# Kernel optimization log

Measured on AMD Instinct MI355X. Metric: run time of the kernel, lower is better.

Reference implementation:

```python
import jax, jax.numpy as jnp
import numpy as np

N_QUBITS = 4
CHROMOSOME = [["rx_gate", "ry_gate", "rz_gate", "h_gate"],
              ["cnot_gate", "cnot_gate", "cnot_gate", "cnot_gate"],
              ["ry_gate", "ry_gate", "ry_gate", "ry_gate"]]

_H = (jnp.array([[1.0, 1.0], [1.0, -1.0]], dtype=jnp.complex64) / jnp.sqrt(2.0).astype(jnp.complex64))


def _ry(t):
    c = jnp.cos(t / 2).astype(jnp.complex64)
    s = jnp.sin(t / 2).astype(jnp.complex64)
    return jnp.stack([jnp.stack([c, -s], -1), jnp.stack([s, c], -1)], -2)


def _rx(t):
    c = jnp.cos(t / 2).astype(jnp.complex64)
    s = (-1j) * jnp.sin(t / 2).astype(jnp.complex64)
    return jnp.stack([jnp.stack([c, s], -1), jnp.stack([s, c], -1)], -2)


def _rz(t):
    e = jnp.exp(-1j * t.astype(jnp.complex64) / 2)
    z = jnp.zeros_like(e)
    return jnp.stack([jnp.stack([e, z], -1), jnp.stack([z, jnp.conj(e)], -1)], -2)


def _apply_1q(state, U, q):
    # state: [N, 2,2,...,2]; U: [2,2] (shared) or [N,2,2] (per-patch encoding)
    s = jnp.moveaxis(state, 1 + q, -1)
    if U.ndim == 3:
        s = jnp.einsum('nab,n...b->n...a', U, s)
    else:
        s = jnp.einsum('ab,n...b->n...a', U, s)
    return jnp.moveaxis(s, -1, 1 + q)


def _cnot(state, c, t):
    s = jnp.moveaxis(state, (1 + c, 1 + t), (-2, -1))
    # control=0 slice unchanged; control=1 slice gets X on target (flip last axis)
    s = jnp.concatenate([s[..., 0:1, :], s[..., 1:2, ::-1]], axis=-2)
    return jnp.moveaxis(s, (-2, -1), (1 + c, 1 + t))


def _simulate(patches, params):
    # patches: [N, n_qubits] real angles in [0,1); params: [n_params]
    N = patches.shape[0]
    state = jnp.zeros((N, 2 ** N_QUBITS), dtype=jnp.complex64).at[:, 0].set(1.0)
    state = state.reshape((N,) + (2,) * N_QUBITS)
    # angle encoding: RY(pi * x_q) on qubit q (encoder='ry' for multichannel path)
    for q in range(N_QUBITS):
        state = _apply_1q(state, _ry(jnp.pi * patches[:, q]), q)
    idx = 0
    for layer in CHROMOSOME:
        for q, g in enumerate(layer):
            if g == 'rx_gate':
                state = _apply_1q(state, _rx(params[idx]), q); idx += 1
            elif g == 'ry_gate':
                state = _apply_1q(state, _ry(params[idx]), q); idx += 1
            elif g == 'rz_gate':
                state = _apply_1q(state, _rz(params[idx]), q); idx += 1
            elif g == 'h_gate':
                state = _apply_1q(state, _H, q)
            elif g == 'cnot_gate':
                state = _cnot(state, q, (q + 1) % N_QUBITS)
    probs = state.real ** 2 + state.imag ** 2  # [N, 2,2,2,2]
    exps = []
    for q in range(N_QUBITS):
        p = jnp.sum(probs, axis=tuple(a for a in range(1, 1 + N_QUBITS) if a != 1 + q))  # [N,2]
        exps.append(p[:, 0] - p[:, 1])  # <Z_q>
    return jnp.stack(exps, -1)  # [N, n_qubits]


def setup_inputs() -> dict:
    key = jax.random.key(0)
    k1, k2 = jax.random.split(key)
    x = jax.random.uniform(k1, (2048, 3, 196, 4), dtype=jnp.float32)
    ansatz_params = jax.random.uniform(k2, (7,), dtype=jnp.float32) * jnp.pi
    return {"x": x, "ansatz_params": ansatz_params}


def reference(x, ansatz_params):
    B, C, P, D = x.shape
    out = _simulate(x.reshape(-1, D), ansatz_params)  # [B*C*P, n_qubits]
    out = out.reshape(B, C, P, N_QUBITS)
    image_size = int((P * N_QUBITS) ** 0.5)  # 28
    # faithful to torch .view(n_images, image_size, image_size, n_channels)
    return out.reshape(B, image_size, image_size, C)
```

## Files before the change

### kernel.cpp

```cpp
#include <hip/hip_runtime.h>


__global__ __launch_bounds__(256) void quanv_kernel(
    const float* __restrict__ x,
    const float* __restrict__ prm,
    float* __restrict__ out,
    int n)
{
    int tid = blockIdx.x * 256 + threadIdx.x;
    if (tid >= n) return;

    float S0, C0, S1, C1, S2, C2;
    __sincosf(prm[0] * 0.5f, &S0, &C0);
    __sincosf(prm[1] * 0.5f, &S1, &C1);
    __sincosf(prm[2] * 0.5f, &S2, &C2);
    float Sf0, Cf0, Sf1, Cf1, Sf2, Cf2, Sf3, Cf3;
    __sincosf(prm[3], &Sf0, &Cf0);
    __sincosf(prm[4], &Sf1, &Cf1);
    __sincosf(prm[5], &Sf2, &Cf2);
    __sincosf(prm[6], &Sf3, &Cf3);

    const float4 xv = reinterpret_cast<const float4*>(x)[tid];

    const float HPI = 1.5707963267948966f;
    float e0s, e0c, e1s, e1c, e2s, e2c, e3s, e3c;
    __sincosf(xv.x * HPI, &e0s, &e0c);
    __sincosf(xv.y * HPI, &e1s, &e1c);
    __sincosf(xv.z * HPI, &e2s, &e2c);
    __sincosf(xv.w * HPI, &e3s, &e3c);

    float v00r = C0 * e0c, v00i = -S0 * e0s;
    float v01r = C0 * e0s, v01i = -S0 * e0c;
    float v10 = C1 * e1c - S1 * e1s;
    float v11 = S1 * e1c + C1 * e1s;
    float v20r = e2c * C2, v20i = -e2c * S2;
    float v21r = e2s * C2, v21i =  e2s * S2;
    const float RS2 = 0.70710678118654752f;
    float v30 = (e3c + e3s) * RS2;
    float v31 = (e3c - e3s) * RS2;

    float t00r = v00r * v10, t00i = v00i * v10;
    float t01r = v00r * v11, t01i = v00i * v11;
    float t10r = v01r * v10, t10i = v01i * v10;
    float t11r = v01r * v11, t11i = v01i * v11;
    float u00r = v20r * v30, u00i = v20i * v30;
    float u01r = v20r * v31, u01i = v20i * v31;
    float u10r = v21r * v30, u10i = v21i * v30;
    float u11r = v21r * v31, u11i = v21i * v31;

#define CMUL(dr, di, ar, ai, br, bi) \
    float dr = (ar) * (br) - (ai) * (bi); \
    float di = (ar) * (bi) + (ai) * (br);
    CMUL(a0r, a0i,  t00r, t00i, u00r, u00i)
    CMUL(a1r, a1i,  t11r, t11i, u01r, u01i)
    CMUL(a2r, a2i,  t00r, t00i, u11r, u11i)
    CMUL(a3r, a3i,  t11r, t11i, u10r, u10i)
    CMUL(a4r, a4i,  t01r, t01i, u10r, u10i)
    CMUL(a5r, a5i,  t10r, t10i, u11r, u11i)
    CMUL(a6r, a6i,  t01r, t01i, u01r, u01i)
    CMUL(a7r, a7i,  t10r, t10i, u00r, u00i)
    CMUL(a8r, a8i,  t11r, t11i, u00r, u00i)
    CMUL(a9r, a9i,  t00r, t00i, u01r, u01i)
    CMUL(a10r, a10i, t11r, t11i, u11r, u11i)
    CMUL(a11r, a11i, t00r, t00i, u10r, u10i)
    CMUL(a12r, a12i, t10r, t10i, u10r, u10i)
    CMUL(a13r, a13i, t01r, t01i, u11r, u11i)
    CMUL(a14r, a14i, t10r, t10i, u01r, u01i)
    CMUL(a15r, a15i, t01r, t01i, u00r, u00i)
#undef CMUL

#define PROB(k) float p##k = a##k##r * a##k##r + a##k##i * a##k##i;
    PROB(0) PROB(1) PROB(2) PROB(3) PROB(4) PROB(5) PROB(6) PROB(7)
    PROB(8) PROB(9) PROB(10) PROB(11) PROB(12) PROB(13) PROB(14) PROB(15)
#undef PROB

    float zpA = (p0 + p1) + (p2 + p3);
    float zpB = (p4 + p5) + (p6 + p7);
    float zpC = (p8 + p9) + (p10 + p11);
    float zpD = (p12 + p13) + (p14 + p15);
    float z0 = (zpA + zpB) - (zpC + zpD);
    float z1 = (zpA + zpC) - (zpB + zpD);
    float z2 = ((p0 + p1) + (p4 + p5) + (p8 + p9) + (p12 + p13))
             - ((p2 + p3) + (p6 + p7) + (p10 + p11) + (p14 + p15));
    float z3 = ((p0 + p2) + (p4 + p6) + (p8 + p10) + (p12 + p14))
             - ((p1 + p3) + (p5 + p7) + (p9 + p11) + (p13 + p15));

#define DOT(m, n) (a##m##r * a##n##r + a##m##i * a##n##i)
    float xs0 = DOT(0, 8) + DOT(1, 9) + DOT(2, 10) + DOT(3, 11)
              + DOT(4, 12) + DOT(5, 13) + DOT(6, 14) + DOT(7, 15);
    float xs1 = DOT(0, 4) + DOT(1, 5) + DOT(2, 6) + DOT(3, 7)
              + DOT(8, 12) + DOT(9, 13) + DOT(10, 14) + DOT(11, 15);
    float xs2 = DOT(0, 2) + DOT(1, 3) + DOT(4, 6) + DOT(5, 7)
              + DOT(8, 10) + DOT(9, 11) + DOT(12, 14) + DOT(13, 15);
    float xs3 = DOT(0, 1) + DOT(2, 3) + DOT(4, 5) + DOT(6, 7)
              + DOT(8, 9) + DOT(10, 11) + DOT(12, 13) + DOT(14, 15);
#undef DOT

    float4 o;
    o.x = Cf0 * z0 - 2.0f * Sf0 * xs0;
    o.y = Cf1 * z1 - 2.0f * Sf1 * xs1;
    o.z = Cf2 * z2 - 2.0f * Sf2 * xs2;
    o.w = Cf3 * z3 - 2.0f * Sf3 * xs3;
    reinterpret_cast<float4*>(out)[tid] = o;
}

extern "C" void kernel_launch(void* const* d_in, const int* in_sizes, int n_in,
                              void* d_out, int out_size, void* d_ws, size_t ws_size,
                              hipStream_t stream) {
    const float* x   = (const float*)d_in[0];
    const float* prm = (const float*)d_in[1];
    float* out = (float*)d_out;
    int n = in_sizes[0] / 4;
    int blocks = (n + 255) / 256;
    quanv_kernel<<<blocks, 256, 0, stream>>>(x, prm, out, n);
}
```

Baseline: 77.34 us.

## Replace statevector simulation with closed-form expectation formulas

```diff
diff --git a/kernel.cpp b/kernel.cpp
--- a/kernel.cpp
+++ b/kernel.cpp
@@ -2,114 +2,63 @@
 
 
 __global__ __launch_bounds__(256) void quanv_kernel(
-    const float* __restrict__ x,
+    const float4* __restrict__ x,
     const float* __restrict__ prm,
-    float* __restrict__ out,
+    float4* __restrict__ out,
     int n)
 {
     int tid = blockIdx.x * 256 + threadIdx.x;
     if (tid >= n) return;
 
-    float S0, C0, S1, C1, S2, C2;
-    __sincosf(prm[0] * 0.5f, &S0, &C0);
-    __sincosf(prm[1] * 0.5f, &S1, &C1);
-    __sincosf(prm[2] * 0.5f, &S2, &C2);
-    float Sf0, Cf0, Sf1, Cf1, Sf2, Cf2, Sf3, Cf3;
-    __sincosf(prm[3], &Sf0, &Cf0);
-    __sincosf(prm[4], &Sf1, &Cf1);
-    __sincosf(prm[5], &Sf2, &Cf2);
-    __sincosf(prm[6], &Sf3, &Cf3);
+    const float INV_2PI = 0.15915494309189535f;
 
-    const float4 xv = reinterpret_cast<const float4*>(x)[tid];
+    float A   = __builtin_amdgcn_cosf(prm[0] * INV_2PI);
+    float Cp1 = __builtin_amdgcn_cosf(prm[1] * INV_2PI);
+    float Sp1 = __builtin_amdgcn_sinf(prm[1] * INV_2PI);
+    float Bc  = __builtin_amdgcn_cosf(prm[2] * INV_2PI);
+    float Cf0 = __builtin_amdgcn_cosf(prm[3] * INV_2PI);
+    float Sf0 = __builtin_amdgcn_sinf(prm[3] * INV_2PI);
+    float Cf1 = __builtin_amdgcn_cosf(prm[4] * INV_2PI);
+    float Sf1 = __builtin_amdgcn_sinf(prm[4] * INV_2PI);
+    float Cf2 = __builtin_amdgcn_cosf(prm[5] * INV_2PI);
+    float Sf2 = __builtin_amdgcn_sinf(prm[5] * INV_2PI);
+    float Cf3 = __builtin_amdgcn_cosf(prm[6] * INV_2PI);
+    float Sf3 = __builtin_amdgcn_sinf(prm[6] * INV_2PI);
 
-    const float HPI = 1.5707963267948966f;
-    float e0s, e0c, e1s, e1c, e2s, e2c, e3s, e3c;
-    __sincosf(xv.x * HPI, &e0s, &e0c);
-    __sincosf(xv.y * HPI, &e1s, &e1c);
-    __sincosf(xv.z * HPI, &e2s, &e2c);
-    __sincosf(xv.w * HPI, &e3s, &e3c);
+    const float4 xv = x[tid];
 
-    float v00r = C0 * e0c, v00i = -S0 * e0s;
-    float v01r = C0 * e0s, v01i = -S0 * e0c;
-    float v10 = C1 * e1c - S1 * e1s;
-    float v11 = S1 * e1c + C1 * e1s;
-    float v20r = e2c * C2, v20i = -e2c * S2;
-    float v21r = e2s * C2, v21i =  e2s * S2;
-    const float RS2 = 0.70710678118654752f;
-    float v30 = (e3c + e3s) * RS2;
-    float v31 = (e3c - e3s) * RS2;
+    float c0 = __builtin_amdgcn_cosf(0.5f * xv.x);
+    float s0 = __builtin_amdgcn_sinf(0.5f * xv.x);
+    float c1 = __builtin_amdgcn_cosf(0.5f * xv.y);
+    float s1 = __builtin_amdgcn_sinf(0.5f * xv.y);
+    float c2 = __builtin_amdgcn_cosf(0.5f * xv.z);
+    float s2 = __builtin_amdgcn_sinf(0.5f * xv.z);
+    float c3 = __builtin_amdgcn_cosf(0.5f * xv.w);
+    float s3 = __builtin_amdgcn_sinf(0.5f * xv.w);
 
-    float t00r = v00r * v10, t00i = v00i * v10;
-    float t01r = v00r * v11, t01i = v00i * v11;
-    float t10r = v01r * v10, t10i = v01i * v10;
-    float t11r = v01r * v11, t11i = v01i * v11;
-    float u00r = v20r * v30, u00i = v20i * v30;
-    float u01r = v20r * v31, u01i = v20i * v31;
-    float u10r = v21r * v30, u10i = v21i * v30;
-    float u11r = v21r * v31, u11i = v21i * v31;
+    float z1 = c1 * Cp1 - s1 * Sp1;
+    float x1 = s1 * Cp1 + c1 * Sp1;
 
-#define CMUL(dr, di, ar, ai, br, bi) \
-    float dr = (ar) * (br) - (ai) * (bi); \
-    float di = (ar) * (bi) + (ai) * (br);
-    CMUL(a0r, a0i,  t00r, t00i, u00r, u00i)
-    CMUL(a1r, a1i,  t11r, t11i, u01r, u01i)
-    CMUL(a2r, a2i,  t00r, t00i, u11r, u11i)
-    CMUL(a3r, a3i,  t11r, t11i, u10r, u10i)
-    CMUL(a4r, a4i,  t01r, t01i, u10r, u10i)
-    CMUL(a5r, a5i,  t10r, t10i, u11r, u11i)
-    CMUL(a6r, a6i,  t01r, t01i, u01r, u01i)
-    CMUL(a7r, a7i,  t10r, t10i, u00r, u00i)
-    CMUL(a8r, a8i,  t11r, t11i, u00r, u00i)
-    CMUL(a9r, a9i,  t00r, t00i, u01r, u01i)
-    CMUL(a10r, a10i, t11r, t11i, u11r, u11i)
-    CMUL(a11r, a11i, t00r, t00i, u10r, u10i)
-    CMUL(a12r, a12i, t10r, t10i, u10r, u10i)
-    CMUL(a13r, a13i, t01r, t01i, u11r, u11i)
-    CMUL(a14r, a14i, t10r, t10i, u01r, u01i)
-    CMUL(a15r, a15i, t01r, t01i, u00r, u00i)
-#undef CMUL
-
-#define PROB(k) float p##k = a##k##r * a##k##r + a##k##i * a##k##i;
-    PROB(0) PROB(1) PROB(2) PROB(3) PROB(4) PROB(5) PROB(6) PROB(7)
-    PROB(8) PROB(9) PROB(10) PROB(11) PROB(12) PROB(13) PROB(14) PROB(15)
-#undef PROB
-
-    float zpA = (p0 + p1) + (p2 + p3);
-    float zpB = (p4 + p5) + (p6 + p7);
-    float zpC = (p8 + p9) + (p10 + p11);
-    float zpD = (p12 + p13) + (p14 + p15);
-    float z0 = (zpA + zpB) - (zpC + zpD);
-    float z1 = (zpA + zpC) - (zpB + zpD);
-    float z2 = ((p0 + p1) + (p4 + p5) + (p8 + p9) + (p12 + p13))
-             - ((p2 + p3) + (p6 + p7) + (p10 + p11) + (p14 + p15));
-    float z3 = ((p0 + p2) + (p4 + p6) + (p8 + p10) + (p12 + p14))
-             - ((p1 + p3) + (p5 + p7) + (p9 + p11) + (p13 + p15));
-
-#define DOT(m, n) (a##m##r * a##n##r + a##m##i * a##n##i)
-    float xs0 = DOT(0, 8) + DOT(1, 9) + DOT(2, 10) + DOT(3, 11)
-              + DOT(4, 12) + DOT(5, 13) + DOT(6, 14) + DOT(7, 15);
-    float xs1 = DOT(0, 4) + DOT(1, 5) + DOT(2, 6) + DOT(3, 7)
-              + DOT(8, 12) + DOT(9, 13) + DOT(10, 14) + DOT(11, 15);
-    float xs2 = DOT(0, 2) + DOT(1, 3) + DOT(4, 6) + DOT(5, 7)
-              + DOT(8, 10) + DOT(9, 11) + DOT(12, 14) + DOT(13, 15);
-    float xs3 = DOT(0, 1) + DOT(2, 3) + DOT(4, 5) + DOT(6, 7)
-              + DOT(8, 9) + DOT(10, 11) + DOT(12, 13) + DOT(14, 15);
-#undef DOT
+    float P = A * c0 * z1;
+    float R = P * c2;
+    float Q = z1 * c2;
+    float T = s0 * x1;
+    float W = Bc * s2;
 
     float4 o;
-    o.x = Cf0 * z0 - 2.0f * Sf0 * xs0;
-    o.y = Cf1 * z1 - 2.0f * Sf1 * xs1;
-    o.z = Cf2 * z2 - 2.0f * Sf2 * xs2;
-    o.w = Cf3 * z3 - 2.0f * Sf3 * xs3;
-    reinterpret_cast<float4*>(out)[tid] = o;
+    o.x = Cf0 * (Q * s3) - Sf0 * T;
+    o.y = Cf1 * P        - Sf1 * (x1 * W);
+    o.z = Cf2 * R        - Sf2 * (W * c3);
+    o.w = Cf3 * (R * s3) - Sf3 * (c3 * T);
+    out[tid] = o;
 }
 
 extern "C" void kernel_launch(void* const* d_in, const int* in_sizes, int n_in,
                               void* d_out, int out_size, void* d_ws, size_t ws_size,
                               hipStream_t stream) {
-    const float* x   = (const float*)d_in[0];
+    const float4* x  = (const float4*)d_in[0];
     const float* prm = (const float*)d_in[1];
-    float* out = (float*)d_out;
+    float4* out = (float4*)d_out;
     int n = in_sizes[0] / 4;
     int blocks = (n + 255) / 256;
     quanv_kernel<<<blocks, 256, 0, stream>>>(x, prm, out, n);
```

Result: faster. 72.14 us (-6.7%).
